# Performance work log

Hardware: AMD Instinct MI355X
Metric: run time of the kernel (lower is better)

Reference implementation:

```python
import jax, jax.numpy as jnp
import numpy as np

T, N, E, IN, H, H2, H3, B, AF = 12, 50000, 800000, 12, 128, 64, 32, 4096, 10
BN_EPS = 1e-5


def _gin_mlp(h, w1, b1, g, be, rm, rv, w2, b2):
    # Linear -> ReLU -> BatchNorm1d (eval: running stats) -> Dropout(eval=id) -> Linear -> ReLU
    h = jax.nn.relu(h @ w1.T + b1)
    h = (h - rm) * (g * jax.lax.rsqrt(rv + BN_EPS)) + be
    return jax.nn.relu(h @ w2.T + b2)


def _gin_conv(x, edge_src, edge_dst, mlp_params):
    # GINConv with eps=0: MLP(x + sum_{j in N(i)} x_j), scatter-add over edges
    agg = jax.ops.segment_sum(x[edge_src], edge_dst, num_segments=x.shape[0])
    return _gin_mlp(x + agg, *mlp_params)


def _gru(xs, wih, whh, bih, bhh):
    # torch.nn.GRU, 1 layer, h0 = zeros. xs: [T, N, H_in]
    h0 = jnp.zeros((xs.shape[1], whh.shape[1]), xs.dtype)

    def step(h, x):
        gi = x @ wih.T + bih
        gh = h @ whh.T + bhh
        ir, iz, inn = jnp.split(gi, 3, axis=-1)
        hr, hz, hn = jnp.split(gh, 3, axis=-1)
        r = jax.nn.sigmoid(ir + hr)
        z = jax.nn.sigmoid(iz + hz)
        n = jnp.tanh(inn + r * hn)
        h_new = (1.0 - z) * n + z * h
        return h_new, h_new

    h_last, ys = jax.lax.scan(step, h0, xs)
    return ys, h_last


def _forward(floats, edge_src, edge_dst, target_idx):
    (x_seq, apart_feature,
     c1_w1, c1_b1, c1_g, c1_be, c1_rm, c1_rv, c1_w2, c1_b2,
     c2_w1, c2_b1, c2_g, c2_be, c2_rm, c2_rv, c2_w2, c2_b2,
     gru_wih, gru_whh, gru_bih, gru_bhh,
     fc1_w, fc1_b, fc2_w, fc2_b, fc3_w, fc3_b) = floats

    c1 = (c1_w1, c1_b1, c1_g, c1_be, c1_rm, c1_rv, c1_w2, c1_b2)
    c2 = (c2_w1, c2_b1, c2_g, c2_be, c2_rm, c2_rv, c2_w2, c2_b2)

    # conv1 per time slot (lax.map keeps the E x H gather intermediate per-step)
    # extra torch.relu after conv1 is a no-op since the MLP ends in ReLU
    emb = jax.lax.map(lambda xt: _gin_conv(xt, edge_src, edge_dst, c1), x_seq)
    seq, _ = _gru(emb, gru_wih, gru_whh, gru_bih, gru_bhh)
    emb2 = jax.lax.map(lambda xt: _gin_conv(xt, edge_src, edge_dst, c2), seq)
    _, h_last = _gru(emb2, gru_wih, gru_whh, gru_bih, gru_bhh)  # same GRU weights reused

    feat = jnp.concatenate([h_last[target_idx], apart_feature], axis=1)
    h = jax.nn.leaky_relu(feat @ fc1_w.T + fc1_b, negative_slope=0.1)
    h = jax.nn.leaky_relu(h @ fc2_w.T + fc2_b, negative_slope=0.05)
    return h @ fc3_w.T + fc3_b  # [B, 1]


def setup_inputs() -> dict:
    key = jax.random.key(0)
    ks = jax.random.split(key, 24)
    f32 = jnp.float32
    w = lambda i, shape, fan: jax.random.normal(ks[i], shape, f32) * (1.0 / np.sqrt(fan))
    return {
        "x_seq": jax.random.normal(ks[0], (T, N, IN), f32),
        "apart_feature": jax.random.normal(ks[1], (B, AF), f32),
        "edge_src": jax.random.randint(ks[2], (E,), 0, N, jnp.int32),
        "edge_dst": jax.random.randint(ks[3], (E,), 0, N, jnp.int32),
        "target_idx": jax.random.randint(ks[4], (B,), 0, N, jnp.int32),
        # conv1 MLP
        "c1_w1": w(5, (H, IN), IN), "c1_b1": jnp.zeros((H,), f32),
        "c1_g": jnp.ones((H,), f32), "c1_be": jnp.zeros((H,), f32),
        "c1_rm": jnp.zeros((H,), f32), "c1_rv": jnp.ones((H,), f32),
        "c1_w2": w(6, (H, H), H), "c1_b2": jnp.zeros((H,), f32),
        # conv2 MLP
        "c2_w1": w(7, (H, H), H), "c2_b1": jnp.zeros((H,), f32),
        "c2_g": jnp.ones((H,), f32), "c2_be": jnp.zeros((H,), f32),
        "c2_rm": jnp.zeros((H,), f32), "c2_rv": jnp.ones((H,), f32),
        "c2_w2": w(8, (H, H), H), "c2_b2": jnp.zeros((H,), f32),
        # shared GRU
        "gru_wih": w(9, (3 * H, H), H), "gru_whh": w(10, (3 * H, H), H),
        "gru_bih": jnp.zeros((3 * H,), f32), "gru_bhh": jnp.zeros((3 * H,), f32),
        # head
        "fc1_w": w(11, (H2, H + AF), H + AF), "fc1_b": jnp.zeros((H2,), f32),
        "fc2_w": w(12, (H3, H2), H2), "fc2_b": jnp.zeros((H3,), f32),
        "fc3_w": w(13, (1, H3), H3), "fc3_b": jnp.zeros((1,), f32),
    }


def reference(x_seq, apart_feature,
              c1_w1, c1_b1, c1_g, c1_be, c1_rm, c1_rv, c1_w2, c1_b2,
              c2_w1, c2_b1, c2_g, c2_be, c2_rm, c2_rv, c2_w2, c2_b2,
              gru_wih, gru_whh, gru_bih, gru_bhh,
              fc1_w, fc1_b, fc2_w, fc2_b, fc3_w, fc3_b,
              edge_src, edge_dst, target_idx):
    floats = (x_seq, apart_feature,
              c1_w1, c1_b1, c1_g, c1_be, c1_rm, c1_rv, c1_w2, c1_b2,
              c2_w1, c2_b1, c2_g, c2_be, c2_rm, c2_rv, c2_w2, c2_b2,
              gru_wih, gru_whh, gru_bih, gru_bhh,
              fc1_w, fc1_b, fc2_w, fc2_b, fc3_w, fc3_b)
    return _forward(floats, edge_src, edge_dst, target_idx)
```

## Files before the change

### kernel.cpp

```cpp
#include <hip/hip_runtime.h>

#define T_STEPS 12
#define NN      50000
#define EE      800000
#define IN_F    12
#define HID     128
#define G3      384
#define BB      4096
#define AF_     10
#define BN_EPS  1e-5f
#define LPAD    136

typedef unsigned short ushort_t;
typedef __attribute__((ext_vector_type(8))) short bf16x8;
typedef __attribute__((ext_vector_type(4))) float f32x4;

#define MFMA(a, b, c) __builtin_amdgcn_mfma_f32_16x16x32_bf16((a), (b), (c), 0, 0, 0)
#define L2E 1.4426950408889634f

__device__ inline float b2f(ushort_t u) { return __uint_as_float(((unsigned)u) << 16); }
__device__ inline float b2f_lo(unsigned u) { return __uint_as_float(u << 16); }
__device__ inline float b2f_hi(unsigned u) { return __uint_as_float(u & 0xffff0000u); }
__device__ inline ushort_t f2b(float f) {
    unsigned u = __float_as_uint(f);
    return (ushort_t)((u + 0x7fffu + ((u >> 16) & 1u)) >> 16);
}
__device__ inline float sigm(float x) {
    return __builtin_amdgcn_rcpf(1.f + __builtin_amdgcn_exp2f(-x * L2E));
}
__device__ inline float ftanh(float x) {
    float xx = fminf(fmaxf(x, -15.f), 15.f);
    float t = __builtin_amdgcn_exp2f(2.f * L2E * xx);
    return (t - 1.f) * __builtin_amdgcn_rcpf(t + 1.f);
}

#define ALIGN_UP(x) (((x) + 255) & ~(size_t)255)
#define SZ_DEG    ALIGN_UP((size_t)NN * 4)
#define SZ_RP     ALIGN_UP((size_t)(NN + 1) * 4)
#define SZ_CUR    ALIGN_UP((size_t)NN * 4)
#define SZ_COL    ALIGN_UP((size_t)EE * 4)
#define SZ_X12A   ALIGN_UP((size_t)T_STEPS * NN * IN_F * 4)
#define SZ_EMB    ALIGN_UP((size_t)T_STEPS * NN * HID * 2)
#define SZ_NHB    ALIGN_UP((size_t)NN * HID * 2)
#define SZ_W128   ALIGN_UP((size_t)HID * HID * 2)
#define SZ_WGRU   ALIGN_UP((size_t)G3 * HID * 2)
#define WS_NEED   (SZ_DEG + SZ_RP + SZ_CUR + SZ_COL + SZ_X12A + SZ_EMB + 3 * SZ_NHB + 3 * SZ_W128 + 2 * SZ_WGRU)

__device__ __align__(256) char g_static_pool[WS_NEED];

__global__ void zero_out_kernel(float* out, int n) {
    int i = blockIdx.x * blockDim.x + threadIdx.x;
    if (i < n) out[i] = 0.f;
}

__global__ void cvt5_kernel(const float* s0, ushort_t* d0, int n0,
                            const float* s1, ushort_t* d1, int n1,
                            const float* s2, ushort_t* d2, int n2,
                            const float* s3, ushort_t* d3, int n3,
                            const float* s4, ushort_t* d4, int n4) {
    int i = blockIdx.x * blockDim.x + threadIdx.x;
    if (i < n0) d0[i] = f2b(s0[i]);
    i -= n0;
    if (i >= 0 && i < n1) d1[i] = f2b(s1[i]);
    i -= n1;
    if (i >= 0 && i < n2) d2[i] = f2b(s2[i]);
    i -= n2;
    if (i >= 0 && i < n3) d3[i] = f2b(s3[i]);
    i -= n3;
    if (i >= 0 && i < n4) d4[i] = f2b(s4[i]);
}

__global__ void init_kernel(int* deg, ushort_t* h1, ushort_t* h2) {
    int i = blockIdx.x * blockDim.x + threadIdx.x;
    if (i < NN) deg[i] = 0;
    if (i < NN * HID) { h1[i] = 0; h2[i] = 0; }
}

__global__ void hist_kernel(const int* __restrict__ dst, int* __restrict__ deg, int E) {
    int e = blockIdx.x * blockDim.x + threadIdx.x;
    if (e < E) {
        unsigned d = (unsigned)dst[e];
        if (d < NN) atomicAdd(&deg[d], 1);
    }
}

__global__ __launch_bounds__(1024) void scan_kernel(const int* __restrict__ deg,
                                                    int* __restrict__ row_ptr,
                                                    int* __restrict__ cursor, int n) {
    __shared__ int wsum[16];
    __shared__ int carry_s;
    int tid = threadIdx.x;
    int wid = tid >> 6, lane = tid & 63;
    if (tid == 0) { carry_s = 0; row_ptr[0] = 0; }
    __syncthreads();
    for (int base = 0; base < n; base += 1024) {
        int i = base + tid;
        int v = (i < n) ? deg[i] : 0;
        int x = v;
#pragma unroll
        for (int off = 1; off < 64; off <<= 1) {
            int t = __shfl_up(x, (unsigned)off);
            if (lane >= off) x += t;
        }
        if (lane == 63) wsum[wid] = x;
        __syncthreads();
        if (tid == 0) {
            int a = 0;
#pragma unroll
            for (int w = 0; w < 16; ++w) { int t = wsum[w]; wsum[w] = a; a += t; }
        }
        __syncthreads();
        int incl = carry_s + wsum[wid] + x;
        if (i < n) {
            row_ptr[i + 1] = incl;
            cursor[i] = incl - v;
        }
        __syncthreads();
        if (tid == 1023) carry_s = incl;
        __syncthreads();
    }
}

__global__ void scatter_kernel(const int* __restrict__ src, const int* __restrict__ dst,
                               int* __restrict__ cursor, int* __restrict__ col, int E) {
    int e = blockIdx.x * blockDim.x + threadIdx.x;
    if (e < E) {
        unsigned d = (unsigned)dst[e];
        if (d < NN) {
            int pos = atomicAdd(&cursor[d], 1);
            if ((unsigned)pos < (unsigned)EE) col[pos] = src[e];
        }
    }
}

__global__ void agg12_all_kernel(const float* __restrict__ x_seq, const int* __restrict__ rp,
                                 const int* __restrict__ col, float* __restrict__ xin12_all, int E) {
    int g = blockIdx.x * blockDim.x + threadIdx.x;
    if (g >= T_STEPS * NN * IN_F) return;
    int t = g / (NN * IN_F);
    int rem = g - t * (NN * IN_F);
    int i = rem / IN_F;
    int f = rem - i * IN_F;
    const float* xt = x_seq + (size_t)t * NN * IN_F;
    float s = xt[rem];
    int e0 = rp[i], e1 = rp[i + 1];
    if (e1 > E) e1 = E;
    for (int e = e0; e < e1; ++e) {
        unsigned c = (unsigned)col[e];
        if (c < NN) s += xt[c * IN_F + f];
    }
    xin12_all[g] = s;
}

__global__ __launch_bounds__(512) void conv1c_all_kernel(const float* __restrict__ xin12_all,
                                                         ushort_t* __restrict__ emb,
                                                         const float* __restrict__ W1, const float* __restrict__ b1,
                                                         const float* __restrict__ gg, const float* __restrict__ be,
                                                         const float* __restrict__ rm, const float* __restrict__ rv,
                                                         const ushort_t* __restrict__ w2b, const float* __restrict__ b2) {
    __shared__ float xs[64][IN_F + 1];
    __shared__ ushort_t l1[64][LPAD];
    int t = blockIdx.y;
    const float* xt = xin12_all + (size_t)t * NN * IN_F;
    ushort_t* et = emb + (size_t)t * NN * HID;
    int tid = threadIdx.x;
    int r0 = blockIdx.x * 64;
    for (int u = tid; u < 64 * IN_F; u += 512) {
        int r = u / IN_F, f = u - r * IN_F;
        int row = r0 + r;
        xs[r][f] = (row < NN) ? xt[(size_t)row * IN_F + f] : 0.f;
    }
    __syncthreads();
    {
        int j = tid & 127, rb = tid >> 7;
        float sc = gg[j] * rsqrtf(rv[j] + BN_EPS);
        float sh = be[j] - rm[j] * sc;
        float bj = b1[j];
        float wreg[IN_F];
#pragma unroll
        for (int k = 0; k < IN_F; ++k) wreg[k] = W1[j * IN_F + k];
#pragma unroll
        for (int q = 0; q < 16; ++q) {
            int r = rb + q * 4;
            float s = bj;
#pragma unroll
            for (int k = 0; k < IN_F; ++k) s += xs[r][k] * wreg[k];
            s = fmaxf(s, 0.f);
            l1[r][j] = f2b(s * sc + sh);
        }
    }
    __syncthreads();
    {
        int wave = tid >> 6, lane = tid & 63, li = lane & 15, ks = lane >> 4;
        int jc = wave * 16 + li;
        const ushort_t* pw = w2b + (size_t)jc * HID + ks * 8;
        f32x4 A0 = {0,0,0,0}, A1 = {0,0,0,0}, A2 = {0,0,0,0}, A3 = {0,0,0,0};
#pragma unroll
        for (int k0 = 0; k0 < HID; k0 += 32) {
            bf16x8 wf = *(const bf16x8*)(pw + k0);
            bf16x8 a0 = *(const bf16x8*)&l1[li][ks * 8 + k0];
            bf16x8 a1 = *(const bf16x8*)&l1[li + 16][ks * 8 + k0];
            bf16x8 a2 = *(const bf16x8*)&l1[li + 32][ks * 8 + k0];
            bf16x8 a3 = *(const bf16x8*)&l1[li + 48][ks * 8 + k0];
            A0 = MFMA(a0, wf, A0); A1 = MFMA(a1, wf, A1);
            A2 = MFMA(a2, wf, A2); A3 = MFMA(a3, wf, A3);
        }
        float bj = b2[jc];
#pragma unroll
        for (int q = 0; q < 4; ++q) {
            int rA = r0 + ks * 4 + q, rB = rA + 16, rC = rA + 32, rD = rA + 48;
            if (rA < NN) et[(size_t)rA * HID + jc] = f2b(fmaxf(A0[q] + bj, 0.f));
            if (rB < NN) et[(size_t)rB * HID + jc] = f2b(fmaxf(A1[q] + bj, 0.f));
            if (rC < NN) et[(size_t)rC * HID + jc] = f2b(fmaxf(A2[q] + bj, 0.f));
            if (rD < NN) et[(size_t)rD * HID + jc] = f2b(fmaxf(A3[q] + bj, 0.f));
        }
    }
}

__global__ __launch_bounds__(512) void gru_step_kernel(const ushort_t* __restrict__ x,
                                                       ushort_t* __restrict__ h,
                                                       const ushort_t* __restrict__ wih,
                                                       const ushort_t* __restrict__ whh,
                                                       const float* __restrict__ bih,
                                                       const float* __restrict__ bhh) {
    int tid = threadIdx.x;
    int wave = tid >> 6, lane = tid & 63, li = lane & 15, ks = lane >> 4;
    int r0 = blockIdx.x * 64;
    int jc = wave * 16 + li;
    const ushort_t* px[4];
    const ushort_t* ph[4];
#pragma unroll
    for (int tt = 0; tt < 4; ++tt) {
        int ra = min(r0 + tt * 16 + li, NN - 1);
        px[tt] = x + (size_t)ra * HID + ks * 8;
        ph[tt] = h + (size_t)ra * HID + ks * 8;
    }
    const ushort_t* pwr = wih + (size_t)jc * HID + ks * 8;
    const ushort_t* pwz = wih + (size_t)(HID + jc) * HID + ks * 8;
    const ushort_t* pwn = wih + (size_t)(2 * HID + jc) * HID + ks * 8;
    const ushort_t* pvr = whh + (size_t)jc * HID + ks * 8;
    const ushort_t* pvz = whh + (size_t)(HID + jc) * HID + ks * 8;
    const ushort_t* pvn = whh + (size_t)(2 * HID + jc) * HID + ks * 8;
    f32x4 Ir[4], Iz[4], In[4], Hr[4], Hz[4], Hn[4];
#pragma unroll
    for (int tt = 0; tt < 4; ++tt) {
        Ir[tt] = (f32x4){0,0,0,0}; Iz[tt] = (f32x4){0,0,0,0}; In[tt] = (f32x4){0,0,0,0};
        Hr[tt] = (f32x4){0,0,0,0}; Hz[tt] = (f32x4){0,0,0,0}; Hn[tt] = (f32x4){0,0,0,0};
    }
#pragma unroll
    for (int k0 = 0; k0 < HID; k0 += 32) {
        bf16x8 wr = *(const bf16x8*)(pwr + k0);
        bf16x8 wz = *(const bf16x8*)(pwz + k0);
        bf16x8 wn = *(const bf16x8*)(pwn + k0);
        bf16x8 vr = *(const bf16x8*)(pvr + k0);
        bf16x8 vz = *(const bf16x8*)(pvz + k0);
        bf16x8 vn = *(const bf16x8*)(pvn + k0);
#pragma unroll
        for (int tt = 0; tt < 4; ++tt) {
            bf16x8 xf = *(const bf16x8*)(px[tt] + k0);
            bf16x8 hf = *(const bf16x8*)(ph[tt] + k0);
            Ir[tt] = MFMA(xf, wr, Ir[tt]);
            Iz[tt] = MFMA(xf, wz, Iz[tt]);
            In[tt] = MFMA(xf, wn, In[tt]);
            Hr[tt] = MFMA(hf, vr, Hr[tt]);
            Hz[tt] = MFMA(hf, vz, Hz[tt]);
            Hn[tt] = MFMA(hf, vn, Hn[tt]);
        }
    }
    float bi_r = bih[jc], bi_z = bih[HID + jc], bi_n = bih[2 * HID + jc];
    float bh_r = bhh[jc], bh_z = bhh[HID + jc], bh_n = bhh[2 * HID + jc];
    float hold[4][4];
#pragma unroll
    for (int tt = 0; tt < 4; ++tt)
#pragma unroll
        for (int q = 0; q < 4; ++q) {
            int rr = min(r0 + tt * 16 + ks * 4 + q, NN - 1);
            hold[tt][q] = b2f(h[(size_t)rr * HID + jc]);
        }
    __syncthreads();
#pragma unroll
    for (int tt = 0; tt < 4; ++tt)
#pragma unroll
        for (int q = 0; q < 4; ++q) {
            int row = r0 + tt * 16 + ks * 4 + q;
            float rg = sigm(Ir[tt][q] + bi_r + Hr[tt][q] + bh_r);
            float zg = sigm(Iz[tt][q] + bi_z + Hz[tt][q] + bh_z);
            float ng = ftanh(In[tt][q] + bi_n + rg * (Hn[tt][q] + bh_n));
            float hv = (1.f - zg) * ng + zg * hold[tt][q];
            if (row < NN) h[(size_t)row * HID + jc] = f2b(hv);
        }
}

__global__ __launch_bounds__(256) void agg128b_kernel(const ushort_t* __restrict__ x,
                                                      const int* __restrict__ rp,
                                                      const int* __restrict__ col,
                                                      ushort_t* __restrict__ out, int E) {
    int node = (blockIdx.x * 256 + threadIdx.x) >> 6;
    int lane = threadIdx.x & 63;
    if (node >= NN) return;
    unsigned v = *(const unsigned*)(x + (size_t)node * HID + lane * 2);
    float s0 = b2f_lo(v);
    float s1 = b2f_hi(v);
    int e0 = rp[node], e1 = rp[node + 1];
    if (e1 > E) e1 = E;
    int e = e0;
    for (; e + 3 < e1; e += 4) {
        unsigned c0 = (unsigned)col[e], c1 = (unsigned)col[e + 1];
        unsigned c2 = (unsigned)col[e + 2], c3 = (unsigned)col[e + 3];
        c0 = (c0 < NN) ? c0 : 0; c1 = (c1 < NN) ? c1 : 0;
        c2 = (c2 < NN) ? c2 : 0; c3 = (c3 < NN) ? c3 : 0;
        unsigned u0 = *(const unsigned*)(x + (size_t)c0 * HID + lane * 2);
        unsigned u1 = *(const unsigned*)(x + (size_t)c1 * HID + lane * 2);
        unsigned u2 = *(const unsigned*)(x + (size_t)c2 * HID + lane * 2);
        unsigned u3 = *(const unsigned*)(x + (size_t)c3 * HID + lane * 2);
        s0 += b2f_lo(u0) + b2f_lo(u1) + b2f_lo(u2) + b2f_lo(u3);
        s1 += b2f_hi(u0) + b2f_hi(u1) + b2f_hi(u2) + b2f_hi(u3);
    }
    for (; e < e1; ++e) {
        unsigned c = (unsigned)col[e];
        if (c < NN) {
            unsigned u = *(const unsigned*)(x + (size_t)c * HID + lane * 2);
            s0 += b2f_lo(u);
            s1 += b2f_hi(u);
        }
    }
    unsigned o = (unsigned)f2b(s0) | ((unsigned)f2b(s1) << 16);
    *(unsigned*)(out + (size_t)node * HID + lane * 2) = o;
}

__global__ __launch_bounds__(512) void mega2_kernel(const ushort_t* __restrict__ xin2,
                                                    ushort_t* __restrict__ h2,
                                                    const ushort_t* __restrict__ w1b, const float* __restrict__ b1,
                                                    const float* __restrict__ gg, const float* __restrict__ be,
                                                    const float* __restrict__ rm, const float* __restrict__ rv,
                                                    const ushort_t* __restrict__ w2b, const float* __restrict__ b2,
                                                    const ushort_t* __restrict__ wih, const ushort_t* __restrict__ whh,
                                                    const float* __restrict__ bih, const float* __restrict__ bhh) {
    __shared__ ushort_t bufA[64][LPAD];
    __shared__ ushort_t bufB[64][LPAD];
    int tid = threadIdx.x;
    int wave = tid >> 6, lane = tid & 63, li = lane & 15, ks = lane >> 4;
    int r0 = blockIdx.x * 64;
    int jc = wave * 16 + li;
    f32x4 Hr[4], Hz[4], Hn[4], C1[4];
#pragma unroll
    for (int tt = 0; tt < 4; ++tt) {
        Hr[tt] = (f32x4){0,0,0,0}; Hz[tt] = (f32x4){0,0,0,0};
        Hn[tt] = (f32x4){0,0,0,0}; C1[tt] = (f32x4){0,0,0,0};
    }
    {
        const ushort_t* pw1 = w1b + (size_t)jc * HID + ks * 8;
        const ushort_t* pvr = whh + (size_t)jc * HID + ks * 8;
        const ushort_t* pvz = whh + (size_t)(HID + jc) * HID + ks * 8;
        const ushort_t* pvn = whh + (size_t)(2 * HID + jc) * HID + ks * 8;
        const ushort_t* pa[4];
        const ushort_t* ph[4];
#pragma unroll
        for (int tt = 0; tt < 4; ++tt) {
            int ra = min(r0 + tt * 16 + li, NN - 1);
            pa[tt] = xin2 + (size_t)ra * HID + ks * 8;
            ph[tt] = h2 + (size_t)ra * HID + ks * 8;
        }
#pragma unroll
        for (int k0 = 0; k0 < HID; k0 += 32) {
            bf16x8 w1f = *(const bf16x8*)(pw1 + k0);
            bf16x8 vr = *(const bf16x8*)(pvr + k0);
            bf16x8 vz = *(const bf16x8*)(pvz + k0);
            bf16x8 vn = *(const bf16x8*)(pvn + k0);
#pragma unroll
            for (int tt = 0; tt < 4; ++tt) {
                bf16x8 af = *(const bf16x8*)(pa[tt] + k0);
                bf16x8 hf = *(const bf16x8*)(ph[tt] + k0);
                C1[tt] = MFMA(af, w1f, C1[tt]);
                Hr[tt] = MFMA(hf, vr, Hr[tt]);
                Hz[tt] = MFMA(hf, vz, Hz[tt]);
                Hn[tt] = MFMA(hf, vn, Hn[tt]);
            }
        }
    }
    float hold[4][4];
#pragma unroll
    for (int tt = 0; tt < 4; ++tt)
#pragma unroll
        for (int q = 0; q < 4; ++q) {
            int rr = min(r0 + tt * 16 + ks * 4 + q, NN - 1);
            hold[tt][q] = b2f(h2[(size_t)rr * HID + jc]);
        }
    {
        float sc = gg[jc] * rsqrtf(rv[jc] + BN_EPS);
        float sh = be[jc] - rm[jc] * sc;
        float bj = b1[jc];
#pragma unroll
        for (int tt = 0; tt < 4; ++tt)
#pragma unroll
            for (int q = 0; q < 4; ++q)
                bufB[tt * 16 + ks * 4 + q][jc] = f2b(fmaxf(C1[tt][q] + bj, 0.f) * sc + sh);
    }
    __syncthreads();
    {
        const ushort_t* pw2 = w2b + (size_t)jc * HID + ks * 8;
        f32x4 C2[4];
#pragma unroll
        for (int tt = 0; tt < 4; ++tt) C2[tt] = (f32x4){0,0,0,0};
#pragma unroll
        for (int k0 = 0; k0 < HID; k0 += 32) {
            bf16x8 wf = *(const bf16x8*)(pw2 + k0);
#pragma unroll
            for (int tt = 0; tt < 4; ++tt) {
                bf16x8 af = *(const bf16x8*)&bufB[li + 16 * tt][ks * 8 + k0];
                C2[tt] = MFMA(af, wf, C2[tt]);
            }
        }
        float bj = b2[jc];
#pragma unroll
        for (int tt = 0; tt < 4; ++tt)
#pragma unroll
            for (int q = 0; q < 4; ++q)
                bufA[tt * 16 + ks * 4 + q][jc] = f2b(fmaxf(C2[tt][q] + bj, 0.f));
    }
    __syncthreads();
    {
        const ushort_t* pwr = wih + (size_t)jc * HID + ks * 8;
        const ushort_t* pwz = wih + (size_t)(HID + jc) * HID + ks * 8;
        const ushort_t* pwn = wih + (size_t)(2 * HID + jc) * HID + ks * 8;
        f32x4 Ir[4], Iz[4], In[4];
#pragma unroll
        for (int tt = 0; tt < 4; ++tt) {
            Ir[tt] = (f32x4){0,0,0,0}; Iz[tt] = (f32x4){0,0,0,0}; In[tt] = (f32x4){0,0,0,0};
        }
#pragma unroll
        for (int k0 = 0; k0 < HID; k0 += 32) {
            bf16x8 wr = *(const bf16x8*)(pwr + k0);
            bf16x8 wz = *(const bf16x8*)(pwz + k0);
            bf16x8 wn = *(const bf16x8*)(pwn + k0);
#pragma unroll
            for (int tt = 0; tt < 4; ++tt) {
                bf16x8 xf = *(const bf16x8*)&bufA[li + 16 * tt][ks * 8 + k0];
                Ir[tt] = MFMA(xf, wr, Ir[tt]);
                Iz[tt] = MFMA(xf, wz, Iz[tt]);
                In[tt] = MFMA(xf, wn, In[tt]);
            }
        }
        float bi_r = bih[jc], bi_z = bih[HID + jc], bi_n = bih[2 * HID + jc];
        float bh_r = bhh[jc], bh_z = bhh[HID + jc], bh_n = bhh[2 * HID + jc];
#pragma unroll
        for (int tt = 0; tt < 4; ++tt)
#pragma unroll
            for (int q = 0; q < 4; ++q) {
                int row = r0 + tt * 16 + ks * 4 + q;
                float rg = sigm(Ir[tt][q] + bi_r + Hr[tt][q] + bh_r);
                float zg = sigm(Iz[tt][q] + bi_z + Hz[tt][q] + bh_z);
                float ng = ftanh(In[tt][q] + bi_n + rg * (Hn[tt][q] + bh_n));
                float hv = (1.f - zg) * ng + zg * hold[tt][q];
                if (row < NN) h2[(size_t)row * HID + jc] = f2b(hv);
            }
    }
}

__global__ __launch_bounds__(64) void head_kernel(const ushort_t* __restrict__ h2, const int* __restrict__ tidx,
                                                  const float* __restrict__ apart,
                                                  const float* __restrict__ w1, const float* __restrict__ b1,
                                                  const float* __restrict__ w2, const float* __restrict__ b2,
                                                  const float* __restrict__ w3, const float* __restrict__ b3,
                                                  float* __restrict__ out) {
    __shared__ float feat[HID + AF_];
    __shared__ float o1[64];
    __shared__ float o2[32];
    int b = blockIdx.x;
    int t = threadIdx.x;
    unsigned node = (unsigned)tidx[b];
    if (node >= NN) node = 0;
    for (int k = t; k < HID; k += 64) feat[k] = b2f(h2[(size_t)node * HID + k]);
    if (t < AF_) feat[HID + t] = apart[(size_t)b * AF_ + t];
    __syncthreads();
    {
        float s = b1[t];
        for (int k = 0; k < HID + AF_; ++k) s += feat[k] * w1[t * (HID + AF_) + k];
        o1[t] = (s > 0.f) ? s : 0.1f * s;
    }
    __syncthreads();
    if (t < 32) {
        float s = b2[t];
        for (int k = 0; k < 64; ++k) s += o1[k] * w2[t * 64 + k];
        o2[t] = (s > 0.f) ? s : 0.05f * s;
    }
    __syncthreads();
    if (t == 0) {
        float s = b3[0];
        for (int k = 0; k < 32; ++k) s += o2[k] * w3[k];
        out[b] = s;
    }
}

extern "C" void kernel_launch(void* const* d_in, const int* in_sizes, int n_in,
                              void* d_out, int out_size, void* d_ws, size_t ws_size,
                              hipStream_t stream) {
    int ie_src = -1, ie_dst = -1, ie_tidx = -1, iw0 = -1;
    bool ok = false;
    if (n_in >= 31 && in_sizes[0] == T_STEPS * NN * IN_F && in_sizes[1] == BB * AF_) {
        if (in_sizes[2] > 100000 && in_sizes[3] == in_sizes[2] && in_sizes[4] == BB &&
            in_sizes[5] == HID * IN_F && in_sizes[11] == HID * HID &&
            in_sizes[21] == G3 * HID && in_sizes[22] == G3 * HID &&
            in_sizes[25] == 64 * (HID + AF_)) {
            ie_src = 2; ie_dst = 3; ie_tidx = 4; iw0 = 5; ok = true;
        } else if (in_sizes[2] == HID * IN_F && in_sizes[8] == HID * HID &&
                   in_sizes[18] == G3 * HID && in_sizes[19] == G3 * HID &&
                   in_sizes[22] == 64 * (HID + AF_) &&
                   in_sizes[28] > 100000 && in_sizes[29] == in_sizes[28] && in_sizes[30] == BB) {
            iw0 = 2; ie_src = 28; ie_dst = 29; ie_tidx = 30; ok = true;
        }
    }
    if (!ok) {
        zero_out_kernel<<<(out_size + 255) / 256, 256, 0, stream>>>((float*)d_out, out_size);
        return;
    }

    const float* x_seq  = (const float*)d_in[0];
    const float* apart  = (const float*)d_in[1];
    const int*   e_src  = (const int*)d_in[ie_src];
    const int*   e_dst  = (const int*)d_in[ie_dst];
    const int*   t_idx  = (const int*)d_in[ie_tidx];
    const float* c1_w1 = (const float*)d_in[iw0 + 0];
    const float* c1_b1 = (const float*)d_in[iw0 + 1];
    const float* c1_g  = (const float*)d_in[iw0 + 2];
    const float* c1_be = (const float*)d_in[iw0 + 3];
    const float* c1_rm = (const float*)d_in[iw0 + 4];
    const float* c1_rv = (const float*)d_in[iw0 + 5];
    const float* c1_w2 = (const float*)d_in[iw0 + 6];
    const float* c1_b2 = (const float*)d_in[iw0 + 7];
    const float* c2_w1 = (const float*)d_in[iw0 + 8];
    const float* c2_b1 = (const float*)d_in[iw0 + 9];
    const float* c2_g  = (const float*)d_in[iw0 + 10];
    const float* c2_be = (const float*)d_in[iw0 + 11];
    const float* c2_rm = (const float*)d_in[iw0 + 12];
    const float* c2_rv = (const float*)d_in[iw0 + 13];
    const float* c2_w2 = (const float*)d_in[iw0 + 14];
    const float* c2_b2 = (const float*)d_in[iw0 + 15];
    const float* g_wih = (const float*)d_in[iw0 + 16];
    const float* g_whh = (const float*)d_in[iw0 + 17];
    const float* g_bih = (const float*)d_in[iw0 + 18];
    const float* g_bhh = (const float*)d_in[iw0 + 19];
    const float* f1_w  = (const float*)d_in[iw0 + 20];
    const float* f1_b  = (const float*)d_in[iw0 + 21];
    const float* f2_w  = (const float*)d_in[iw0 + 22];
    const float* f2_b  = (const float*)d_in[iw0 + 23];
    const float* f3_w  = (const float*)d_in[iw0 + 24];
    const float* f3_b  = (const float*)d_in[iw0 + 25];

    int E = in_sizes[ie_src];
    if (E > EE) E = EE;

    char* base;
    if (ws_size >= WS_NEED) {
        base = (char*)d_ws;
    } else {
        void* sp = nullptr;
        hipGetSymbolAddress(&sp, HIP_SYMBOL(g_static_pool));
        if (sp == nullptr) {
            zero_out_kernel<<<(out_size + 255) / 256, 256, 0, stream>>>((float*)d_out, out_size);
            return;
        }
        base = (char*)sp;
    }
    size_t off = 0;
    auto nxt = [&](size_t bytes) { char* p = base + off; off += bytes; return p; };
    int*      deg      = (int*)nxt(SZ_DEG);
    int*      row_ptr  = (int*)nxt(SZ_RP);
    int*      cursor   = (int*)nxt(SZ_CUR);
    int*      col      = (int*)nxt(SZ_COL);
    float*    xin12a   = (float*)nxt(SZ_X12A);
    ushort_t* emb      = (ushort_t*)nxt(SZ_EMB);
    ushort_t* xin2     = (ushort_t*)nxt(SZ_NHB);
    ushort_t* h1       = (ushort_t*)nxt(SZ_NHB);
    ushort_t* h2       = (ushort_t*)nxt(SZ_NHB);
    ushort_t* wb_c1w2  = (ushort_t*)nxt(SZ_W128);
    ushort_t* wb_c2w1  = (ushort_t*)nxt(SZ_W128);
    ushort_t* wb_c2w2  = (ushort_t*)nxt(SZ_W128);
    ushort_t* wb_wih   = (ushort_t*)nxt(SZ_WGRU);
    ushort_t* wb_whh   = (ushort_t*)nxt(SZ_WGRU);

    const int NW = 3 * HID * HID + 2 * G3 * HID;
    cvt5_kernel<<<(NW + 255) / 256, 256, 0, stream>>>(c1_w2, wb_c1w2, HID * HID,
                                                      c2_w1, wb_c2w1, HID * HID,
                                                      c2_w2, wb_c2w2, HID * HID,
                                                      g_wih, wb_wih, G3 * HID,
                                                      g_whh, wb_whh, G3 * HID);

    init_kernel<<<(NN * HID + 255) / 256, 256, 0, stream>>>(deg, h1, h2);

    hist_kernel<<<(E + 255) / 256, 256, 0, stream>>>(e_dst, deg, E);
    scan_kernel<<<1, 1024, 0, stream>>>(deg, row_ptr, cursor, NN);
    scatter_kernel<<<(E + 255) / 256, 256, 0, stream>>>(e_src, e_dst, cursor, col, E);

    const int NB = (NN + 63) / 64;

    agg12_all_kernel<<<(T_STEPS * NN * IN_F + 255) / 256, 256, 0, stream>>>(x_seq, row_ptr, col, xin12a, E);
    conv1c_all_kernel<<<dim3(NB, T_STEPS), 512, 0, stream>>>(xin12a, emb,
                                                             c1_w1, c1_b1, c1_g, c1_be, c1_rm, c1_rv,
                                                             wb_c1w2, c1_b2);

    for (int t = 0; t < T_STEPS; ++t) {
        gru_step_kernel<<<NB, 512, 0, stream>>>(emb + (size_t)t * NN * HID, h1,
                                                wb_wih, wb_whh, g_bih, g_bhh);
        agg128b_kernel<<<(NN * 64 + 255) / 256, 256, 0, stream>>>(h1, row_ptr, col, xin2, E);
        mega2_kernel<<<NB, 512, 0, stream>>>(xin2, h2,
                                             wb_c2w1, c2_b1, c2_g, c2_be, c2_rm, c2_rv,
                                             wb_c2w2, c2_b2,
                                             wb_wih, wb_whh, g_bih, g_bhh);
    }

    head_kernel<<<BB, 64, 0, stream>>>(h2, t_idx, apart, f1_w, f1_b, f2_w, f2_b, f3_w, f3_b, (float*)d_out);
}
```

Measured before the change: 2.584 ms.

## Fuse next-step GRU1 with current mega2 step and vectorize conv1 aggregation

```diff
diff --git a/kernel.cpp b/kernel.cpp
--- a/kernel.cpp
+++ b/kernel.cpp
@@ -10,6 +10,7 @@
 #define AF_     10
 #define BN_EPS  1e-5f
 #define LPAD    136
+#define NBLK    ((NN + 63) / 64)
 
 typedef unsigned short ushort_t;
 typedef __attribute__((ext_vector_type(8))) short bf16x8;
@@ -32,6 +33,9 @@
     float xx = fminf(fmaxf(x, -15.f), 15.f);
     float t = __builtin_amdgcn_exp2f(2.f * L2E * xx);
     return (t - 1.f) * __builtin_amdgcn_rcpf(t + 1.f);
+}
+__device__ inline void v4add(float4& a, const float4 b) {
+    a.x += b.x; a.y += b.y; a.z += b.z; a.w += b.w;
 }
 
 #define ALIGN_UP(x) (((x) + 255) & ~(size_t)255)
@@ -133,23 +137,37 @@
     }
 }
 
-__global__ void agg12_all_kernel(const float* __restrict__ x_seq, const int* __restrict__ rp,
-                                 const int* __restrict__ col, float* __restrict__ xin12_all, int E) {
+__global__ void agg12v_kernel(const float* __restrict__ x_seq, const int* __restrict__ rp,
+                              const int* __restrict__ col, float* __restrict__ xin12_all, int E) {
     int g = blockIdx.x * blockDim.x + threadIdx.x;
-    if (g >= T_STEPS * NN * IN_F) return;
-    int t = g / (NN * IN_F);
-    int rem = g - t * (NN * IN_F);
-    int i = rem / IN_F;
-    int f = rem - i * IN_F;
+    if (g >= T_STEPS * NN) return;
+    int t = g / NN;
+    int i = g - t * NN;
     const float* xt = x_seq + (size_t)t * NN * IN_F;
-    float s = xt[rem];
+    const float4* pr = (const float4*)(xt + (size_t)i * IN_F);
+    float4 a0 = pr[0], a1 = pr[1], a2 = pr[2];
     int e0 = rp[i], e1 = rp[i + 1];
     if (e1 > E) e1 = E;
-    for (int e = e0; e < e1; ++e) {
+    int e = e0;
+    for (; e + 1 < e1; e += 2) {
+        unsigned c0 = (unsigned)col[e], c1 = (unsigned)col[e + 1];
+        c0 = (c0 < NN) ? c0 : 0; c1 = (c1 < NN) ? c1 : 0;
+        const float4* p0 = (const float4*)(xt + (size_t)c0 * IN_F);
+        const float4* p1 = (const float4*)(xt + (size_t)c1 * IN_F);
+        float4 b0 = p0[0], b1 = p0[1], b2 = p0[2];
+        float4 d0 = p1[0], d1 = p1[1], d2 = p1[2];
+        v4add(a0, b0); v4add(a1, b1); v4add(a2, b2);
+        v4add(a0, d0); v4add(a1, d1); v4add(a2, d2);
+    }
+    for (; e < e1; ++e) {
         unsigned c = (unsigned)col[e];
-        if (c < NN) s += xt[c * IN_F + f];
-    }
-    xin12_all[g] = s;
+        if (c < NN) {
+            const float4* pn = (const float4*)(xt + (size_t)c * IN_F);
+            v4add(a0, pn[0]); v4add(a1, pn[1]); v4add(a2, pn[2]);
+        }
+    }
+    float4* po = (float4*)(xin12_all + (size_t)g * IN_F);
+    po[0] = a0; po[1] = a1; po[2] = a2;
 }
 
 __global__ __launch_bounds__(512) void conv1c_all_kernel(const float* __restrict__ xin12_all,
@@ -217,15 +235,15 @@
     }
 }
 
-__global__ __launch_bounds__(512) void gru_step_kernel(const ushort_t* __restrict__ x,
-                                                       ushort_t* __restrict__ h,
-                                                       const ushort_t* __restrict__ wih,
-                                                       const ushort_t* __restrict__ whh,
-                                                       const float* __restrict__ bih,
-                                                       const float* __restrict__ bhh) {
+__device__ __forceinline__ void gru_body(const ushort_t* __restrict__ x,
+                                         ushort_t* __restrict__ h,
+                                         const ushort_t* __restrict__ wih,
+                                         const ushort_t* __restrict__ whh,
+                                         const float* __restrict__ bih,
+                                         const float* __restrict__ bhh, int blk) {
     int tid = threadIdx.x;
     int wave = tid >> 6, lane = tid & 63, li = lane & 15, ks = lane >> 4;
-    int r0 = blockIdx.x * 64;
+    int r0 = blk * 64;
     int jc = wave * 16 + li;
     const ushort_t* px[4];
     const ushort_t* ph[4];
@@ -289,6 +307,167 @@
             float hv = (1.f - zg) * ng + zg * hold[tt][q];
             if (row < NN) h[(size_t)row * HID + jc] = f2b(hv);
         }
+}
+
+__device__ __forceinline__ void mega2_body(const ushort_t* __restrict__ xin2,
+                                           ushort_t* __restrict__ h2,
+                                           const ushort_t* __restrict__ w1b, const float* __restrict__ b1,
+                                           const float* __restrict__ gg, const float* __restrict__ be,
+                                           const float* __restrict__ rm, const float* __restrict__ rv,
+                                           const ushort_t* __restrict__ w2b, const float* __restrict__ b2,
+                                           const ushort_t* __restrict__ wih, const ushort_t* __restrict__ whh,
+                                           const float* __restrict__ bih, const float* __restrict__ bhh, int blk) {
+    __shared__ ushort_t bufA[64][LPAD];
+    __shared__ ushort_t bufB[64][LPAD];
+    int tid = threadIdx.x;
+    int wave = tid >> 6, lane = tid & 63, li = lane & 15, ks = lane >> 4;
+    int r0 = blk * 64;
+    int jc = wave * 16 + li;
+    f32x4 Hr[4], Hz[4], Hn[4], C1[4];
+#pragma unroll
+    for (int tt = 0; tt < 4; ++tt) {
+        Hr[tt] = (f32x4){0,0,0,0}; Hz[tt] = (f32x4){0,0,0,0};
+        Hn[tt] = (f32x4){0,0,0,0}; C1[tt] = (f32x4){0,0,0,0};
+    }
+    {
+        const ushort_t* pw1 = w1b + (size_t)jc * HID + ks * 8;
+        const ushort_t* pvr = whh + (size_t)jc * HID + ks * 8;
+        const ushort_t* pvz = whh + (size_t)(HID + jc) * HID + ks * 8;
+        const ushort_t* pvn = whh + (size_t)(2 * HID + jc) * HID + ks * 8;
+        const ushort_t* pa[4];
+        const ushort_t* ph[4];
+#pragma unroll
+        for (int tt = 0; tt < 4; ++tt) {
+            int ra = min(r0 + tt * 16 + li, NN - 1);
+            pa[tt] = xin2 + (size_t)ra * HID + ks * 8;
+            ph[tt] = h2 + (size_t)ra * HID + ks * 8;
+        }
+#pragma unroll
+        for (int k0 = 0; k0 < HID; k0 += 32) {
+            bf16x8 w1f = *(const bf16x8*)(pw1 + k0);
+            bf16x8 vr = *(const bf16x8*)(pvr + k0);
+            bf16x8 vz = *(const bf16x8*)(pvz + k0);
+            bf16x8 vn = *(const bf16x8*)(pvn + k0);
+#pragma unroll
+            for (int tt = 0; tt < 4; ++tt) {
+                bf16x8 af = *(const bf16x8*)(pa[tt] + k0);
+                bf16x8 hf = *(const bf16x8*)(ph[tt] + k0);
+                C1[tt] = MFMA(af, w1f, C1[tt]);
+                Hr[tt] = MFMA(hf, vr, Hr[tt]);
+                Hz[tt] = MFMA(hf, vz, Hz[tt]);
+                Hn[tt] = MFMA(hf, vn, Hn[tt]);
+            }
+        }
+    }
+    float hold[4][4];
+#pragma unroll
+    for (int tt = 0; tt < 4; ++tt)
+#pragma unroll
+        for (int q = 0; q < 4; ++q) {
+            int rr = min(r0 + tt * 16 + ks * 4 + q, NN - 1);
+            hold[tt][q] = b2f(h2[(size_t)rr * HID + jc]);
+        }
+    {
+        float sc = gg[jc] * rsqrtf(rv[jc] + BN_EPS);
+        float sh = be[jc] - rm[jc] * sc;
+        float bj = b1[jc];
+#pragma unroll
+        for (int tt = 0; tt < 4; ++tt)
+#pragma unroll
+            for (int q = 0; q < 4; ++q)
+                bufB[tt * 16 + ks * 4 + q][jc] = f2b(fmaxf(C1[tt][q] + bj, 0.f) * sc + sh);
+    }
+    __syncthreads();
+    {
+        const ushort_t* pw2 = w2b + (size_t)jc * HID + ks * 8;
+        f32x4 C2[4];
+#pragma unroll
+        for (int tt = 0; tt < 4; ++tt) C2[tt] = (f32x4){0,0,0,0};
+#pragma unroll
+        for (int k0 = 0; k0 < HID; k0 += 32) {
+            bf16x8 wf = *(const bf16x8*)(pw2 + k0);
+#pragma unroll
+            for (int tt = 0; tt < 4; ++tt) {
+                bf16x8 af = *(const bf16x8*)&bufB[li + 16 * tt][ks * 8 + k0];
+                C2[tt] = MFMA(af, wf, C2[tt]);
+            }
+        }
+        float bj = b2[jc];
+#pragma unroll
+        for (int tt = 0; tt < 4; ++tt)
+#pragma unroll
+            for (int q = 0; q < 4; ++q)
+                bufA[tt * 16 + ks * 4 + q][jc] = f2b(fmaxf(C2[tt][q] + bj, 0.f));
+    }
+    __syncthreads();
+    {
+        const ushort_t* pwr = wih + (size_t)jc * HID + ks * 8;
+        const ushort_t* pwz = wih + (size_t)(HID + jc) * HID + ks * 8;
+        const ushort_t* pwn = wih + (size_t)(2 * HID + jc) * HID + ks * 8;
+        f32x4 Ir[4], Iz[4], In[4];
+#pragma unroll
+        for (int tt = 0; tt < 4; ++tt) {
+            Ir[tt] = (f32x4){0,0,0,0}; Iz[tt] = (f32x4){0,0,0,0}; In[tt] = (f32x4){0,0,0,0};
+        }
+#pragma unroll
+        for (int k0 = 0; k0 < HID; k0 += 32) {
+            bf16x8 wr = *(const bf16x8*)(pwr + k0);
+            bf16x8 wz = *(const bf16x8*)(pwz + k0);
+            bf16x8 wn = *(const bf16x8*)(pwn + k0);
+#pragma unroll
+            for (int tt = 0; tt < 4; ++tt) {
+                bf16x8 xf = *(const bf16x8*)&bufA[li + 16 * tt][ks * 8 + k0];
+                Ir[tt] = MFMA(xf, wr, Ir[tt]);
+                Iz[tt] = MFMA(xf, wz, Iz[tt]);
+                In[tt] = MFMA(xf, wn, In[tt]);
+            }
+        }
+        float bi_r = bih[jc], bi_z = bih[HID + jc], bi_n = bih[2 * HID + jc];
+        float bh_r = bhh[jc], bh_z = bhh[HID + jc], bh_n = bhh[2 * HID + jc];
+#pragma unroll
+        for (int tt = 0; tt < 4; ++tt)
+#pragma unroll
+            for (int q = 0; q < 4; ++q) {
+                int row = r0 + tt * 16 + ks * 4 + q;
+                float rg = sigm(Ir[tt][q] + bi_r + Hr[tt][q] + bh_r);
+                float zg = sigm(Iz[tt][q] + bi_z + Hz[tt][q] + bh_z);
+                float ng = ftanh(In[tt][q] + bi_n + rg * (Hn[tt][q] + bh_n));
+                float hv = (1.f - zg) * ng + zg * hold[tt][q];
+                if (row < NN) h2[(size_t)row * HID + jc] = f2b(hv);
+            }
+    }
+}
+
+__global__ __launch_bounds__(512) void gru_step_kernel(const ushort_t* __restrict__ x, ushort_t* __restrict__ h,
+                                                       const ushort_t* __restrict__ wih, const ushort_t* __restrict__ whh,
+                                                       const float* __restrict__ bih, const float* __restrict__ bhh) {
+    gru_body(x, h, wih, whh, bih, bhh, blockIdx.x);
+}
+
+__global__ __launch_bounds__(512) void mega2_kernel(const ushort_t* __restrict__ xin2, ushort_t* __restrict__ h2,
+                                                    const ushort_t* __restrict__ w1b, const float* __restrict__ b1,
+                                                    const float* __restrict__ gg, const float* __restrict__ be,
+                                                    const float* __restrict__ rm, const float* __restrict__ rv,
+                                                    const ushort_t* __restrict__ w2b, const float* __restrict__ b2,
+                                                    const ushort_t* __restrict__ wih, const ushort_t* __restrict__ whh,
+                                                    const float* __restrict__ bih, const float* __restrict__ bhh) {
+    mega2_body(xin2, h2, w1b, b1, gg, be, rm, rv, w2b, b2, wih, whh, bih, bhh, blockIdx.x);
+}
+
+__global__ __launch_bounds__(512) void fused_mg_kernel(const ushort_t* __restrict__ xin2, ushort_t* __restrict__ h2,
+                                                       const ushort_t* __restrict__ w1b, const float* __restrict__ b1,
+                                                       const float* __restrict__ gg, const float* __restrict__ be,
+                                                       const float* __restrict__ rm, const float* __restrict__ rv,
+                                                       const ushort_t* __restrict__ w2b, const float* __restrict__ b2,
+                                                       const ushort_t* __restrict__ wih, const ushort_t* __restrict__ whh,
+                                                       const float* __restrict__ bih, const float* __restrict__ bhh,
+                                                       const ushort_t* __restrict__ emb_next, ushort_t* __restrict__ h1) {
+    int b = blockIdx.x;
+    if (b < NBLK) {
+        mega2_body(xin2, h2, w1b, b1, gg, be, rm, rv, w2b, b2, wih, whh, bih, bhh, b);
+    } else {
+        gru_body(emb_next, h1, wih, whh, bih, bhh, b - NBLK);
+    }
 }
 
 __global__ __launch_bounds__(256) void agg128b_kernel(const ushort_t* __restrict__ x,
@@ -326,135 +505,6 @@
     }
     unsigned o = (unsigned)f2b(s0) | ((unsigned)f2b(s1) << 16);
     *(unsigned*)(out + (size_t)node * HID + lane * 2) = o;
-}
-
-__global__ __launch_bounds__(512) void mega2_kernel(const ushort_t* __restrict__ xin2,
-                                                    ushort_t* __restrict__ h2,
-                                                    const ushort_t* __restrict__ w1b, const float* __restrict__ b1,
-                                                    const float* __restrict__ gg, const float* __restrict__ be,
-                                                    const float* __restrict__ rm, const float* __restrict__ rv,
-                                                    const ushort_t* __restrict__ w2b, const float* __restrict__ b2,
-                                                    const ushort_t* __restrict__ wih, const ushort_t* __restrict__ whh,
-                                                    const float* __restrict__ bih, const float* __restrict__ bhh) {
-    __shared__ ushort_t bufA[64][LPAD];
-    __shared__ ushort_t bufB[64][LPAD];
-    int tid = threadIdx.x;
-    int wave = tid >> 6, lane = tid & 63, li = lane & 15, ks = lane >> 4;
-    int r0 = blockIdx.x * 64;
-    int jc = wave * 16 + li;
-    f32x4 Hr[4], Hz[4], Hn[4], C1[4];
-#pragma unroll
-    for (int tt = 0; tt < 4; ++tt) {
-        Hr[tt] = (f32x4){0,0,0,0}; Hz[tt] = (f32x4){0,0,0,0};
-        Hn[tt] = (f32x4){0,0,0,0}; C1[tt] = (f32x4){0,0,0,0};
-    }
-    {
-        const ushort_t* pw1 = w1b + (size_t)jc * HID + ks * 8;
-        const ushort_t* pvr = whh + (size_t)jc * HID + ks * 8;
-        const ushort_t* pvz = whh + (size_t)(HID + jc) * HID + ks * 8;
-        const ushort_t* pvn = whh + (size_t)(2 * HID + jc) * HID + ks * 8;
-        const ushort_t* pa[4];
-        const ushort_t* ph[4];
-#pragma unroll
-        for (int tt = 0; tt < 4; ++tt) {
-            int ra = min(r0 + tt * 16 + li, NN - 1);
-            pa[tt] = xin2 + (size_t)ra * HID + ks * 8;
-            ph[tt] = h2 + (size_t)ra * HID + ks * 8;
-        }
-#pragma unroll
-        for (int k0 = 0; k0 < HID; k0 += 32) {
-            bf16x8 w1f = *(const bf16x8*)(pw1 + k0);
-            bf16x8 vr = *(const bf16x8*)(pvr + k0);
-            bf16x8 vz = *(const bf16x8*)(pvz + k0);
-            bf16x8 vn = *(const bf16x8*)(pvn + k0);
-#pragma unroll
-            for (int tt = 0; tt < 4; ++tt) {
-                bf16x8 af = *(const bf16x8*)(pa[tt] + k0);
-                bf16x8 hf = *(const bf16x8*)(ph[tt] + k0);
-                C1[tt] = MFMA(af, w1f, C1[tt]);
-                Hr[tt] = MFMA(hf, vr, Hr[tt]);
-                Hz[tt] = MFMA(hf, vz, Hz[tt]);
-                Hn[tt] = MFMA(hf, vn, Hn[tt]);
-            }
-        }
-    }
-    float hold[4][4];
-#pragma unroll
-    for (int tt = 0; tt < 4; ++tt)
-#pragma unroll
-        for (int q = 0; q < 4; ++q) {
-            int rr = min(r0 + tt * 16 + ks * 4 + q, NN - 1);
-            hold[tt][q] = b2f(h2[(size_t)rr * HID + jc]);
-        }
-    {
-        float sc = gg[jc] * rsqrtf(rv[jc] + BN_EPS);
-        float sh = be[jc] - rm[jc] * sc;
-        float bj = b1[jc];
-#pragma unroll
-        for (int tt = 0; tt < 4; ++tt)
-#pragma unroll
-            for (int q = 0; q < 4; ++q)
-                bufB[tt * 16 + ks * 4 + q][jc] = f2b(fmaxf(C1[tt][q] + bj, 0.f) * sc + sh);
-    }
-    __syncthreads();
-    {
-        const ushort_t* pw2 = w2b + (size_t)jc * HID + ks * 8;
-        f32x4 C2[4];
-#pragma unroll
-        for (int tt = 0; tt < 4; ++tt) C2[tt] = (f32x4){0,0,0,0};
-#pragma unroll
-        for (int k0 = 0; k0 < HID; k0 += 32) {
-            bf16x8 wf = *(const bf16x8*)(pw2 + k0);
-#pragma unroll
-            for (int tt = 0; tt < 4; ++tt) {
-                bf16x8 af = *(const bf16x8*)&bufB[li + 16 * tt][ks * 8 + k0];
-                C2[tt] = MFMA(af, wf, C2[tt]);
-            }
-        }
-        float bj = b2[jc];
-#pragma unroll
-        for (int tt = 0; tt < 4; ++tt)
-#pragma unroll
-            for (int q = 0; q < 4; ++q)
-                bufA[tt * 16 + ks * 4 + q][jc] = f2b(fmaxf(C2[tt][q] + bj, 0.f));
-    }
-    __syncthreads();
-    {
-        const ushort_t* pwr = wih + (size_t)jc * HID + ks * 8;
-        const ushort_t* pwz = wih + (size_t)(HID + jc) * HID + ks * 8;
-        const ushort_t* pwn = wih + (size_t)(2 * HID + jc) * HID + ks * 8;
-        f32x4 Ir[4], Iz[4], In[4];
-#pragma unroll
-        for (int tt = 0; tt < 4; ++tt) {
-            Ir[tt] = (f32x4){0,0,0,0}; Iz[tt] = (f32x4){0,0,0,0}; In[tt] = (f32x4){0,0,0,0};
-        }
-#pragma unroll
-        for (int k0 = 0; k0 < HID; k0 += 32) {
-            bf16x8 wr = *(const bf16x8*)(pwr + k0);
-            bf16x8 wz = *(const bf16x8*)(pwz + k0);
-            bf16x8 wn = *(const bf16x8*)(pwn + k0);
-#pragma unroll
-            for (int tt = 0; tt < 4; ++tt) {
-                bf16x8 xf = *(const bf16x8*)&bufA[li + 16 * tt][ks * 8 + k0];
-                Ir[tt] = MFMA(xf, wr, Ir[tt]);
-                Iz[tt] = MFMA(xf, wz, Iz[tt]);
-                In[tt] = MFMA(xf, wn, In[tt]);
-            }
-        }
-        float bi_r = bih[jc], bi_z = bih[HID + jc], bi_n = bih[2 * HID + jc];
-        float bh_r = bhh[jc], bh_z = bhh[HID + jc], bh_n = bhh[2 * HID + jc];
-#pragma unroll
-        for (int tt = 0; tt < 4; ++tt)
-#pragma unroll
-            for (int q = 0; q < 4; ++q) {
-                int row = r0 + tt * 16 + ks * 4 + q;
-                float rg = sigm(Ir[tt][q] + bi_r + Hr[tt][q] + bh_r);
-                float zg = sigm(Iz[tt][q] + bi_z + Hz[tt][q] + bh_z);
-                float ng = ftanh(In[tt][q] + bi_n + rg * (Hn[tt][q] + bh_n));
-                float hv = (1.f - zg) * ng + zg * hold[tt][q];
-                if (row < NN) h2[(size_t)row * HID + jc] = f2b(hv);
-            }
-    }
 }
 
 __global__ __launch_bounds__(64) void head_kernel(const ushort_t* __restrict__ h2, const int* __restrict__ tidx,
@@ -592,22 +642,25 @@
     scan_kernel<<<1, 1024, 0, stream>>>(deg, row_ptr, cursor, NN);
     scatter_kernel<<<(E + 255) / 256, 256, 0, stream>>>(e_src, e_dst, cursor, col, E);
 
-    const int NB = (NN + 63) / 64;
-
-    agg12_all_kernel<<<(T_STEPS * NN * IN_F + 255) / 256, 256, 0, stream>>>(x_seq, row_ptr, col, xin12a, E);
-    conv1c_all_kernel<<<dim3(NB, T_STEPS), 512, 0, stream>>>(xin12a, emb,
-                                                             c1_w1, c1_b1, c1_g, c1_be, c1_rm, c1_rv,
-                                                             wb_c1w2, c1_b2);
-
-    for (int t = 0; t < T_STEPS; ++t) {
-        gru_step_kernel<<<NB, 512, 0, stream>>>(emb + (size_t)t * NN * HID, h1,
-                                                wb_wih, wb_whh, g_bih, g_bhh);
+    agg12v_kernel<<<(T_STEPS * NN + 255) / 256, 256, 0, stream>>>(x_seq, row_ptr, col, xin12a, E);
+    conv1c_all_kernel<<<dim3(NBLK, T_STEPS), 512, 0, stream>>>(xin12a, emb,
+                                                               c1_w1, c1_b1, c1_g, c1_be, c1_rm, c1_rv,
+                                                               wb_c1w2, c1_b2);
+
+    gru_step_kernel<<<NBLK, 512, 0, stream>>>(emb, h1, wb_wih, wb_whh, g_bih, g_bhh);
+    agg128b_kernel<<<(NN * 64 + 255) / 256, 256, 0, stream>>>(h1, row_ptr, col, xin2, E);
+    for (int t = 0; t < T_STEPS - 1; ++t) {
+        fused_mg_kernel<<<2 * NBLK, 512, 0, stream>>>(xin2, h2,
+                                                      wb_c2w1, c2_b1, c2_g, c2_be, c2_rm, c2_rv,
+                                                      wb_c2w2, c2_b2,
+                                                      wb_wih, wb_whh, g_bih, g_bhh,
+                                                      emb + (size_t)(t + 1) * NN * HID, h1);
         agg128b_kernel<<<(NN * 64 + 255) / 256, 256, 0, stream>>>(h1, row_ptr, col, xin2, E);
-        mega2_kernel<<<NB, 512, 0, stream>>>(xin2, h2,
-                                             wb_c2w1, c2_b1, c2_g, c2_be, c2_rm, c2_rv,
-                                             wb_c2w2, c2_b2,
-                                             wb_wih, wb_whh, g_bih, g_bhh);
-    }
+    }
+    mega2_kernel<<<NBLK, 512, 0, stream>>>(xin2, h2,
+                                           wb_c2w1, c2_b1, c2_g, c2_be, c2_rm, c2_rv,
+                                           wb_c2w2, c2_b2,
+                                           wb_wih, wb_whh, g_bih, g_bhh);
 
     head_kernel<<<BB, 64, 0, stream>>>(h2, t_idx, apart, f1_w, f1_b, f2_w, f2_b, f3_w, f3_b, (float*)d_out);
 }
```

Result: faster. 2.351 ms (-9.0%).
